# Performance work log

Hardware: AMD Instinct MI355X
Metric: run time of the kernel (lower is better)

## Reference

```python
import jax, jax.numpy as jnp
import numpy as np

HIDDEN = 2560
NUM_HEADS = 8
NUM_KV_HEADS = 1
HEAD_DIM = 512  # is_full=True -> HEAD_DIM_FULL
MAX_HD = 512
SCALE = 1.0 / float(HEAD_DIM) ** 0.5
SEQ = 32768
SLIDE = 512
CUR_POS = 4000
RING_POS = 100


def setup_inputs() -> dict:
    key = jax.random.key(0)
    ks = jax.random.split(key, 7)
    x = jax.random.normal(ks[0], (1, HIDDEN, 1, 1), jnp.float32)
    kv_full = jax.random.normal(ks[1], (2, NUM_KV_HEADS, SEQ, MAX_HD), jnp.float32) * 0.02
    kv_sliding = jax.random.normal(ks[2], (2, NUM_KV_HEADS, SLIDE, MAX_HD), jnp.float32) * 0.02
    wq = jax.random.normal(ks[3], (NUM_HEADS * HEAD_DIM, HIDDEN), jnp.float32) * 0.02
    wk = jax.random.normal(ks[4], (NUM_KV_HEADS * HEAD_DIM, HIDDEN), jnp.float32) * 0.02
    wv = jax.random.normal(ks[5], (NUM_KV_HEADS * HEAD_DIM, HIDDEN), jnp.float32) * 0.02
    wo = jax.random.normal(ks[6], (HIDDEN, NUM_HEADS * HEAD_DIM), jnp.float32) * 0.02
    return {"x": x, "kv_sliding": kv_sliding, "kv_full": kv_full,
            "wq": wq, "wk": wk, "wv": wv, "wo": wo,
            "current_pos": CUR_POS, "ring_pos": RING_POS}


def reference(x, kv_sliding, kv_full, wq, wk, wv, wo, current_pos, ring_pos):
    # 1x1 convs on a [1,C,1,1] input are plain matvecs
    xv = x.reshape(HIDDEN)
    q = (wq @ xv).reshape(NUM_HEADS, HEAD_DIM)            # [H, D]
    k = (wk @ xv).reshape(NUM_KV_HEADS, HEAD_DIM)         # [1, D]
    v = (wv @ xv).reshape(NUM_KV_HEADS, HEAD_DIM)         # [1, D]
    # is_full=True, slot_idx=0: slice-update write into kv_full at current_pos
    kv_full = jax.lax.dynamic_update_slice(
        kv_full, k[None, :, None, :].astype(kv_full.dtype), (0, 0, current_pos, 0))
    kv_full = jax.lax.dynamic_update_slice(
        kv_full, v[None, :, None, :].astype(kv_full.dtype), (1, 0, current_pos, 0))
    k_cache = kv_full[0, 0, :, :HEAD_DIM]                 # [S, D]
    v_cache = kv_full[1, 0, :, :HEAD_DIM]                 # [S, D]
    # GQA with 1 kv head: repeat == broadcast across the H query heads
    scores = jnp.einsum('hd,sd->hs', q.astype(jnp.float32),
                        k_cache.astype(jnp.float32)) * SCALE   # [H, S]
    probs = jax.nn.softmax(scores, axis=-1)
    attn = jnp.einsum('hs,sd->hd', probs,
                      v_cache.astype(jnp.float32)).astype(x.dtype)  # [H, D]
    out = (wo @ attn.reshape(NUM_HEADS * HEAD_DIM)).reshape(1, HIDDEN, 1, 1)
    return out
```

## Files before the change

### kernel.cpp

```cpp
#include <hip/hip_runtime.h>
#include <stdint.h>

#define HIDDEN 2560
#define NHEADS 8
#define HD 512
#define QDIM (NHEADS * HD)
#define SEQ 32768
#define CHUNK 64
#define NCHUNK (SEQ / CHUNK)
#define PART_ST (8 + NHEADS * HD)
#define SCALE 0.044194173824159216f

#define WS_QKV 0
#define WS_K   4096
#define WS_V   4608
#define WS_ATT 8192
#define WS_PART 16384

__global__ __launch_bounds__(256) void qkv_gemv(
    const float* __restrict__ x,
    const float* __restrict__ wq,
    const float* __restrict__ wk,
    const float* __restrict__ wv,
    float* __restrict__ qkv) {
  const int row = blockIdx.x * 4 + (threadIdx.x >> 6);
  const int lane = threadIdx.x & 63;
  const float* w;
  if (row < QDIM) w = wq + (size_t)row * HIDDEN;
  else if (row < QDIM + HD) w = wk + (size_t)(row - QDIM) * HIDDEN;
  else w = wv + (size_t)(row - QDIM - HD) * HIDDEN;
  float acc = 0.f;
#pragma unroll
  for (int i = 0; i < 5; i++) {
    const int j = i * 512 + lane * 8;
    float4 a0 = *(const float4*)(w + j);
    float4 a1 = *(const float4*)(w + j + 4);
    float4 b0 = *(const float4*)(x + j);
    float4 b1 = *(const float4*)(x + j + 4);
    acc += a0.x * b0.x + a0.y * b0.y + a0.z * b0.z + a0.w * b0.w +
           a1.x * b1.x + a1.y * b1.y + a1.z * b1.z + a1.w * b1.w;
  }
#pragma unroll
  for (int off = 32; off > 0; off >>= 1) acc += __shfl_xor(acc, off);
  if (lane == 0) qkv[row] = acc;
}

__global__ __launch_bounds__(256) void attn_partial(
    const float* __restrict__ kvfull,
    const float* __restrict__ ws,
    const int* __restrict__ cur_pos,
    float* __restrict__ part) {
  __shared__ float sc[CHUNK][NHEADS];
  __shared__ float4 vtmp[NHEADS][128];
  const int tid = threadIdx.x;
  const int lane = tid & 63;
  const int wid = tid >> 6;
  const int cur = cur_pos[0];
  const int s0 = blockIdx.x * CHUNK;
  const float* K = kvfull;
  const float* V = kvfull + (size_t)SEQ * HD;

  float qf[NHEADS][8];
#pragma unroll
  for (int h = 0; h < NHEADS; h++) {
    float4 a = *(const float4*)(ws + WS_QKV + h * HD + lane * 8);
    float4 b = *(const float4*)(ws + WS_QKV + h * HD + lane * 8 + 4);
    qf[h][0] = a.x; qf[h][1] = a.y; qf[h][2] = a.z; qf[h][3] = a.w;
    qf[h][4] = b.x; qf[h][5] = b.y; qf[h][6] = b.z; qf[h][7] = b.w;
  }

  for (int ii = 0; ii < CHUNK / 4; ii++) {
    const int scix = wid * (CHUNK / 4) + ii;
    const int s = s0 + scix;
    const float* krow = (s == cur) ? (ws + WS_K) : (K + (size_t)s * HD);
    float4 a = *(const float4*)(krow + lane * 8);
    float4 b = *(const float4*)(krow + lane * 8 + 4);
    float kb[8] = {a.x, a.y, a.z, a.w, b.x, b.y, b.z, b.w};
    float p[NHEADS];
#pragma unroll
    for (int h = 0; h < NHEADS; h++) {
      float t = 0.f;
#pragma unroll
      for (int e = 0; e < 8; e++) t += kb[e] * qf[h][e];
      p[h] = t;
    }
#pragma unroll
    for (int off = 32; off > 0; off >>= 1) {
#pragma unroll
      for (int h = 0; h < NHEADS; h++) p[h] += __shfl_xor(p[h], off);
    }
    if (lane == 0) {
#pragma unroll
      for (int h = 0; h < NHEADS; h++) sc[scix][h] = __expf(p[h] * SCALE);
    }
  }
  __syncthreads();

  float* pb = part + (size_t)blockIdx.x * PART_ST;
  if (tid < NHEADS) {
    float lsum = 0.f;
    for (int s = 0; s < CHUNK; s++) lsum += sc[s][tid];
    pb[tid] = lsum;
  }

  const int g = tid >> 7;
  const int tl = tid & 127;
  const int d0 = tl * 4;
  float4 acc[NHEADS];
#pragma unroll
  for (int h = 0; h < NHEADS; h++) acc[h] = make_float4(0.f, 0.f, 0.f, 0.f);
  for (int sy = g * (CHUNK / 2); sy < (g + 1) * (CHUNK / 2); sy++) {
    const int s = s0 + sy;
    const float* vrow = (s == cur) ? (ws + WS_V) : (V + (size_t)s * HD);
    float4 v4 = *(const float4*)(vrow + d0);
#pragma unroll
    for (int h = 0; h < NHEADS; h++) {
      const float pp = sc[sy][h];
      acc[h].x += pp * v4.x; acc[h].y += pp * v4.y;
      acc[h].z += pp * v4.z; acc[h].w += pp * v4.w;
    }
  }
  if (g == 1) {
#pragma unroll
    for (int h = 0; h < NHEADS; h++) vtmp[h][tl] = acc[h];
  }
  __syncthreads();
  if (g == 0) {
#pragma unroll
    for (int h = 0; h < NHEADS; h++) {
      float4 o = vtmp[h][tl];
      o.x += acc[h].x; o.y += acc[h].y; o.z += acc[h].z; o.w += acc[h].w;
      *(float4*)(pb + 8 + h * HD + d0) = o;
    }
  }
}

__global__ __launch_bounds__(256) void attn_reduce(
    const float* __restrict__ part,
    float* __restrict__ attn) {
  const int h = blockIdx.x >> 4;
  const int dgrp = blockIdx.x & 15;
  const int tid = threadIdx.x;
  __shared__ float red[256];
  __shared__ float pacc[8][32];

  red[tid] = part[(size_t)tid * PART_ST + h] + part[(size_t)(tid + 256) * PART_ST + h];
  __syncthreads();
  for (int off = 128; off > 0; off >>= 1) {
    if (tid < off) red[tid] += red[tid + off];
    __syncthreads();
  }
  const float Linv = 1.f / red[0];

  const int dloc = tid & 31;
  const int bs = tid >> 5;
  const int d = dgrp * 32 + dloc;
  float acc = 0.f;
#pragma unroll 8
  for (int b = bs * (NCHUNK / 8); b < (bs + 1) * (NCHUNK / 8); b++) {
    acc += part[(size_t)b * PART_ST + 8 + h * HD + d];
  }
  pacc[bs][dloc] = acc;
  __syncthreads();
  if (tid < 32) {
    float s = ((pacc[0][tid] + pacc[1][tid]) + (pacc[2][tid] + pacc[3][tid])) +
              ((pacc[4][tid] + pacc[5][tid]) + (pacc[6][tid] + pacc[7][tid]));
    attn[h * HD + dgrp * 32 + tid] = s * Linv;
  }
}

__global__ __launch_bounds__(256) void out_gemv(
    const float* __restrict__ wo,
    const float* __restrict__ attn,
    float* __restrict__ out) {
  const int row = blockIdx.x * 4 + (threadIdx.x >> 6);
  const int lane = threadIdx.x & 63;
  const float* w = wo + (size_t)row * QDIM;
  float acc = 0.f;
#pragma unroll
  for (int i = 0; i < 8; i++) {
    const int j = i * 512 + lane * 8;
    float4 w0 = *(const float4*)(w + j);
    float4 w1 = *(const float4*)(w + j + 4);
    float4 a0 = *(const float4*)(attn + j);
    float4 a1 = *(const float4*)(attn + j + 4);
    acc += w0.x * a0.x + w0.y * a0.y + w0.z * a0.z + w0.w * a0.w +
           w1.x * a1.x + w1.y * a1.y + w1.z * a1.z + w1.w * a1.w;
  }
#pragma unroll
  for (int off = 32; off > 0; off >>= 1) acc += __shfl_xor(acc, off);
  if (lane == 0) out[row] = acc;
}

extern "C" void kernel_launch(void* const* d_in, const int* in_sizes, int n_in,
                              void* d_out, int out_size, void* d_ws, size_t ws_size,
                              hipStream_t stream) {
  (void)in_sizes; (void)n_in; (void)out_size; (void)ws_size;
  const float* x      = (const float*)d_in[0];
  const float* kvfull = (const float*)d_in[2];
  const float* wq     = (const float*)d_in[3];
  const float* wk     = (const float*)d_in[4];
  const float* wv     = (const float*)d_in[5];
  const float* wo     = (const float*)d_in[6];
  const int* cur_pos  = (const int*)d_in[7];
  float* out = (float*)d_out;
  float* ws = (float*)d_ws;

  qkv_gemv<<<(QDIM + 2 * HD) / 4, 256, 0, stream>>>(x, wq, wk, wv, ws + WS_QKV);
  attn_partial<<<NCHUNK, 256, 0, stream>>>(kvfull, ws, cur_pos, ws + WS_PART);
  attn_reduce<<<NHEADS * 16, 256, 0, stream>>>(ws + WS_PART, ws + WS_ATT);
  out_gemv<<<HIDDEN / 4, 256, 0, stream>>>(wo, ws + WS_ATT, out);
}
```

Measured before the change: 282.2 us.

## Fuse four attention-decode kernels into one cooperative persistent kernel with grid syncs

```diff
diff --git a/kernel.cpp b/kernel.cpp
--- a/kernel.cpp
+++ b/kernel.cpp
@@ -1,4 +1,5 @@
 #include <hip/hip_runtime.h>
+#include <hip/hip_cooperative_groups.h>
 #include <stdint.h>
 
 #define HIDDEN 2560
@@ -6,190 +7,202 @@
 #define HD 512
 #define QDIM (NHEADS * HD)
 #define SEQ 32768
-#define CHUNK 64
+#define CHUNK 128
 #define NCHUNK (SEQ / CHUNK)
-#define PART_ST (8 + NHEADS * HD)
+#define PART_ST (8 + QDIM)
 #define SCALE 0.044194173824159216f
-
-#define WS_QKV 0
-#define WS_K   4096
-#define WS_V   4608
-#define WS_ATT 8192
+#define NBLK 256
+#define NTHR 256
+
+#define WS_Q    0
+#define WS_K    4096
+#define WS_V    4608
+#define WS_ATT  8192
 #define WS_PART 16384
 
-__global__ __launch_bounds__(256) void qkv_gemv(
+__global__ __launch_bounds__(NTHR) void fused_attn(
     const float* __restrict__ x,
+    const float* __restrict__ kvfull,
     const float* __restrict__ wq,
     const float* __restrict__ wk,
     const float* __restrict__ wv,
-    float* __restrict__ qkv) {
-  const int row = blockIdx.x * 4 + (threadIdx.x >> 6);
-  const int lane = threadIdx.x & 63;
-  const float* w;
-  if (row < QDIM) w = wq + (size_t)row * HIDDEN;
-  else if (row < QDIM + HD) w = wk + (size_t)(row - QDIM) * HIDDEN;
-  else w = wv + (size_t)(row - QDIM - HD) * HIDDEN;
-  float acc = 0.f;
-#pragma unroll
-  for (int i = 0; i < 5; i++) {
-    const int j = i * 512 + lane * 8;
-    float4 a0 = *(const float4*)(w + j);
-    float4 a1 = *(const float4*)(w + j + 4);
-    float4 b0 = *(const float4*)(x + j);
-    float4 b1 = *(const float4*)(x + j + 4);
-    acc += a0.x * b0.x + a0.y * b0.y + a0.z * b0.z + a0.w * b0.w +
-           a1.x * b1.x + a1.y * b1.y + a1.z * b1.z + a1.w * b1.w;
-  }
-#pragma unroll
-  for (int off = 32; off > 0; off >>= 1) acc += __shfl_xor(acc, off);
-  if (lane == 0) qkv[row] = acc;
-}
-
-__global__ __launch_bounds__(256) void attn_partial(
-    const float* __restrict__ kvfull,
-    const float* __restrict__ ws,
+    const float* __restrict__ wo,
     const int* __restrict__ cur_pos,
-    float* __restrict__ part) {
-  __shared__ float sc[CHUNK][NHEADS];
-  __shared__ float4 vtmp[NHEADS][128];
+    float* __restrict__ ws,
+    float* __restrict__ out) {
+  namespace cg = cooperative_groups;
+  cg::grid_group grid = cg::this_grid();
+
   const int tid = threadIdx.x;
   const int lane = tid & 63;
   const int wid = tid >> 6;
-  const int cur = cur_pos[0];
-  const int s0 = blockIdx.x * CHUNK;
-  const float* K = kvfull;
-  const float* V = kvfull + (size_t)SEQ * HD;
-
-  float qf[NHEADS][8];
-#pragma unroll
-  for (int h = 0; h < NHEADS; h++) {
-    float4 a = *(const float4*)(ws + WS_QKV + h * HD + lane * 8);
-    float4 b = *(const float4*)(ws + WS_QKV + h * HD + lane * 8 + 4);
-    qf[h][0] = a.x; qf[h][1] = a.y; qf[h][2] = a.z; qf[h][3] = a.w;
-    qf[h][4] = b.x; qf[h][5] = b.y; qf[h][6] = b.z; qf[h][7] = b.w;
-  }
-
-  for (int ii = 0; ii < CHUNK / 4; ii++) {
-    const int scix = wid * (CHUNK / 4) + ii;
-    const int s = s0 + scix;
-    const float* krow = (s == cur) ? (ws + WS_K) : (K + (size_t)s * HD);
-    float4 a = *(const float4*)(krow + lane * 8);
-    float4 b = *(const float4*)(krow + lane * 8 + 4);
-    float kb[8] = {a.x, a.y, a.z, a.w, b.x, b.y, b.z, b.w};
-    float p[NHEADS];
+  const int b = blockIdx.x;
+  const int gw = b * 4 + wid;
+
+  __shared__ float sc[CHUNK * NHEADS];
+  __shared__ float4 vtmp[NHEADS * 128];
+  __shared__ float sLinv;
+
+  for (int r = gw; r < QDIM + 2 * HD; r += 4 * NBLK) {
+    const float* w;
+    if (r < QDIM) w = wq + (size_t)r * HIDDEN;
+    else if (r < QDIM + HD) w = wk + (size_t)(r - QDIM) * HIDDEN;
+    else w = wv + (size_t)(r - QDIM - HD) * HIDDEN;
+    float acc = 0.f;
+#pragma unroll
+    for (int i = 0; i < 5; i++) {
+      const int j = i * 512 + lane * 8;
+      float4 a0 = *(const float4*)(w + j);
+      float4 a1 = *(const float4*)(w + j + 4);
+      float4 b0 = *(const float4*)(x + j);
+      float4 b1 = *(const float4*)(x + j + 4);
+      acc += a0.x * b0.x + a0.y * b0.y + a0.z * b0.z + a0.w * b0.w +
+             a1.x * b1.x + a1.y * b1.y + a1.z * b1.z + a1.w * b1.w;
+    }
+#pragma unroll
+    for (int off = 32; off > 0; off >>= 1) acc += __shfl_xor(acc, off);
+    if (lane == 0) ws[WS_Q + r] = acc;
+  }
+
+  grid.sync();
+
+  {
+    const int cur = cur_pos[0];
+    const float* K = kvfull;
+    const float* V = kvfull + (size_t)SEQ * HD;
+    const int s0 = b * CHUNK;
+
+    float qf[NHEADS][8];
 #pragma unroll
     for (int h = 0; h < NHEADS; h++) {
-      float t = 0.f;
-#pragma unroll
-      for (int e = 0; e < 8; e++) t += kb[e] * qf[h][e];
-      p[h] = t;
-    }
-#pragma unroll
-    for (int off = 32; off > 0; off >>= 1) {
-#pragma unroll
-      for (int h = 0; h < NHEADS; h++) p[h] += __shfl_xor(p[h], off);
-    }
-    if (lane == 0) {
-#pragma unroll
-      for (int h = 0; h < NHEADS; h++) sc[scix][h] = __expf(p[h] * SCALE);
-    }
-  }
-  __syncthreads();
-
-  float* pb = part + (size_t)blockIdx.x * PART_ST;
-  if (tid < NHEADS) {
-    float lsum = 0.f;
-    for (int s = 0; s < CHUNK; s++) lsum += sc[s][tid];
-    pb[tid] = lsum;
-  }
-
-  const int g = tid >> 7;
-  const int tl = tid & 127;
-  const int d0 = tl * 4;
-  float4 acc[NHEADS];
-#pragma unroll
-  for (int h = 0; h < NHEADS; h++) acc[h] = make_float4(0.f, 0.f, 0.f, 0.f);
-  for (int sy = g * (CHUNK / 2); sy < (g + 1) * (CHUNK / 2); sy++) {
-    const int s = s0 + sy;
-    const float* vrow = (s == cur) ? (ws + WS_V) : (V + (size_t)s * HD);
-    float4 v4 = *(const float4*)(vrow + d0);
-#pragma unroll
-    for (int h = 0; h < NHEADS; h++) {
-      const float pp = sc[sy][h];
-      acc[h].x += pp * v4.x; acc[h].y += pp * v4.y;
-      acc[h].z += pp * v4.z; acc[h].w += pp * v4.w;
-    }
-  }
-  if (g == 1) {
-#pragma unroll
-    for (int h = 0; h < NHEADS; h++) vtmp[h][tl] = acc[h];
-  }
-  __syncthreads();
-  if (g == 0) {
-#pragma unroll
-    for (int h = 0; h < NHEADS; h++) {
-      float4 o = vtmp[h][tl];
-      o.x += acc[h].x; o.y += acc[h].y; o.z += acc[h].z; o.w += acc[h].w;
-      *(float4*)(pb + 8 + h * HD + d0) = o;
-    }
-  }
-}
-
-__global__ __launch_bounds__(256) void attn_reduce(
-    const float* __restrict__ part,
-    float* __restrict__ attn) {
-  const int h = blockIdx.x >> 4;
-  const int dgrp = blockIdx.x & 15;
-  const int tid = threadIdx.x;
-  __shared__ float red[256];
-  __shared__ float pacc[8][32];
-
-  red[tid] = part[(size_t)tid * PART_ST + h] + part[(size_t)(tid + 256) * PART_ST + h];
-  __syncthreads();
-  for (int off = 128; off > 0; off >>= 1) {
-    if (tid < off) red[tid] += red[tid + off];
-    __syncthreads();
-  }
-  const float Linv = 1.f / red[0];
-
-  const int dloc = tid & 31;
-  const int bs = tid >> 5;
-  const int d = dgrp * 32 + dloc;
-  float acc = 0.f;
-#pragma unroll 8
-  for (int b = bs * (NCHUNK / 8); b < (bs + 1) * (NCHUNK / 8); b++) {
-    acc += part[(size_t)b * PART_ST + 8 + h * HD + d];
-  }
-  pacc[bs][dloc] = acc;
-  __syncthreads();
-  if (tid < 32) {
-    float s = ((pacc[0][tid] + pacc[1][tid]) + (pacc[2][tid] + pacc[3][tid])) +
-              ((pacc[4][tid] + pacc[5][tid]) + (pacc[6][tid] + pacc[7][tid]));
-    attn[h * HD + dgrp * 32 + tid] = s * Linv;
-  }
-}
-
-__global__ __launch_bounds__(256) void out_gemv(
-    const float* __restrict__ wo,
-    const float* __restrict__ attn,
-    float* __restrict__ out) {
-  const int row = blockIdx.x * 4 + (threadIdx.x >> 6);
-  const int lane = threadIdx.x & 63;
-  const float* w = wo + (size_t)row * QDIM;
-  float acc = 0.f;
-#pragma unroll
-  for (int i = 0; i < 8; i++) {
-    const int j = i * 512 + lane * 8;
-    float4 w0 = *(const float4*)(w + j);
-    float4 w1 = *(const float4*)(w + j + 4);
-    float4 a0 = *(const float4*)(attn + j);
-    float4 a1 = *(const float4*)(attn + j + 4);
-    acc += w0.x * a0.x + w0.y * a0.y + w0.z * a0.z + w0.w * a0.w +
-           w1.x * a1.x + w1.y * a1.y + w1.z * a1.z + w1.w * a1.w;
-  }
-#pragma unroll
-  for (int off = 32; off > 0; off >>= 1) acc += __shfl_xor(acc, off);
-  if (lane == 0) out[row] = acc;
+      float4 a = *(const float4*)(ws + WS_Q + h * HD + lane * 8);
+      float4 c = *(const float4*)(ws + WS_Q + h * HD + lane * 8 + 4);
+      qf[h][0] = a.x; qf[h][1] = a.y; qf[h][2] = a.z; qf[h][3] = a.w;
+      qf[h][4] = c.x; qf[h][5] = c.y; qf[h][6] = c.z; qf[h][7] = c.w;
+    }
+
+    for (int ii = 0; ii < CHUNK / 4; ii++) {
+      const int scix = wid * (CHUNK / 4) + ii;
+      const int s = s0 + scix;
+      const float* krow = (s == cur) ? (ws + WS_K) : (K + (size_t)s * HD);
+      float4 a = *(const float4*)(krow + lane * 8);
+      float4 c = *(const float4*)(krow + lane * 8 + 4);
+      float kb[8] = {a.x, a.y, a.z, a.w, c.x, c.y, c.z, c.w};
+      float p[NHEADS];
+#pragma unroll
+      for (int h = 0; h < NHEADS; h++) {
+        float t = 0.f;
+#pragma unroll
+        for (int e = 0; e < 8; e++) t += kb[e] * qf[h][e];
+        p[h] = t;
+      }
+#pragma unroll
+      for (int off = 32; off > 0; off >>= 1) {
+#pragma unroll
+        for (int h = 0; h < NHEADS; h++) p[h] += __shfl_xor(p[h], off);
+      }
+      if (lane == 0) {
+#pragma unroll
+        for (int h = 0; h < NHEADS; h++) sc[scix * NHEADS + h] = __expf(p[h] * SCALE);
+      }
+    }
+    __syncthreads();
+
+    float* pb = ws + WS_PART + (size_t)b * PART_ST;
+    {
+      const int h0 = wid * 2;
+      float s1 = sc[lane * NHEADS + h0]     + sc[(64 + lane) * NHEADS + h0];
+      float s2 = sc[lane * NHEADS + h0 + 1] + sc[(64 + lane) * NHEADS + h0 + 1];
+#pragma unroll
+      for (int off = 32; off > 0; off >>= 1) {
+        s1 += __shfl_xor(s1, off);
+        s2 += __shfl_xor(s2, off);
+      }
+      if (lane == 0) { pb[h0] = s1; pb[h0 + 1] = s2; }
+    }
+
+    const int g = tid >> 7;
+    const int tl = tid & 127;
+    const int d0 = tl * 4;
+    float4 acc8[NHEADS];
+#pragma unroll
+    for (int h = 0; h < NHEADS; h++) acc8[h] = make_float4(0.f, 0.f, 0.f, 0.f);
+    for (int sy = g * (CHUNK / 2); sy < (g + 1) * (CHUNK / 2); sy++) {
+      const int s = s0 + sy;
+      const float* vrow = (s == cur) ? (ws + WS_V) : (V + (size_t)s * HD);
+      float4 v4 = *(const float4*)(vrow + d0);
+#pragma unroll
+      for (int h = 0; h < NHEADS; h++) {
+        const float pp = sc[sy * NHEADS + h];
+        acc8[h].x += pp * v4.x; acc8[h].y += pp * v4.y;
+        acc8[h].z += pp * v4.z; acc8[h].w += pp * v4.w;
+      }
+    }
+    if (g == 1) {
+#pragma unroll
+      for (int h = 0; h < NHEADS; h++) vtmp[h * 128 + tl] = acc8[h];
+    }
+    __syncthreads();
+    if (g == 0) {
+#pragma unroll
+      for (int h = 0; h < NHEADS; h++) {
+        float4 o = vtmp[h * 128 + tl];
+        o.x += acc8[h].x; o.y += acc8[h].y; o.z += acc8[h].z; o.w += acc8[h].w;
+        *(float4*)(pb + 8 + h * HD + d0) = o;
+      }
+    }
+  }
+
+  grid.sync();
+
+  {
+    const int h = b >> 5;
+    const float* part = ws + WS_PART;
+    if (wid == 0) {
+      float d_ = 0.f;
+#pragma unroll
+      for (int q4 = 0; q4 < 4; q4++)
+        d_ += part[(size_t)(q4 * 64 + lane) * PART_ST + h];
+#pragma unroll
+      for (int off = 32; off > 0; off >>= 1) d_ += __shfl_xor(d_, off);
+      if (lane == 0) sLinv = 1.f / d_;
+    }
+    const int dim = tid & 15;
+    const int bg = tid >> 4;
+    const int dl = (b * 16 + dim) & (HD - 1);
+    float a_ = 0.f;
+    for (int bb = bg * 16; bb < bg * 16 + 16; bb++)
+      a_ += part[(size_t)bb * PART_ST + 8 + h * HD + dl];
+    __syncthreads();
+    sc[tid] = a_;
+    __syncthreads();
+    if (tid < 16) {
+      float s_ = 0.f;
+#pragma unroll
+      for (int q4 = 0; q4 < 16; q4++) s_ += sc[q4 * 16 + tid];
+      ws[WS_ATT + b * 16 + tid] = s_ * sLinv;
+    }
+  }
+
+  grid.sync();
+
+  for (int r = gw; r < HIDDEN; r += 4 * NBLK) {
+    const float* w = wo + (size_t)r * QDIM;
+    float acc = 0.f;
+#pragma unroll
+    for (int i = 0; i < 8; i++) {
+      const int j = i * 512 + lane * 8;
+      float4 w0 = *(const float4*)(w + j);
+      float4 w1 = *(const float4*)(w + j + 4);
+      float4 a0 = *(const float4*)(ws + WS_ATT + j);
+      float4 a1 = *(const float4*)(ws + WS_ATT + j + 4);
+      acc += w0.x * a0.x + w0.y * a0.y + w0.z * a0.z + w0.w * a0.w +
+             w1.x * a1.x + w1.y * a1.y + w1.z * a1.z + w1.w * a1.w;
+    }
+#pragma unroll
+    for (int off = 32; off > 0; off >>= 1) acc += __shfl_xor(acc, off);
+    if (lane == 0) out[r] = acc;
+  }
 }
 
 extern "C" void kernel_launch(void* const* d_in, const int* in_sizes, int n_in,
@@ -206,8 +219,8 @@
   float* out = (float*)d_out;
   float* ws = (float*)d_ws;
 
-  qkv_gemv<<<(QDIM + 2 * HD) / 4, 256, 0, stream>>>(x, wq, wk, wv, ws + WS_QKV);
-  attn_partial<<<NCHUNK, 256, 0, stream>>>(kvfull, ws, cur_pos, ws + WS_PART);
-  attn_reduce<<<NHEADS * 16, 256, 0, stream>>>(ws + WS_PART, ws + WS_ATT);
-  out_gemv<<<HIDDEN / 4, 256, 0, stream>>>(wo, ws + WS_ATT, out);
+  void* args[] = {(void*)&x, (void*)&kvfull, (void*)&wq, (void*)&wk, (void*)&wv,
+                  (void*)&wo, (void*)&cur_pos, (void*)&ws, (void*)&out};
+  hipLaunchCooperativeKernel((void*)fused_attn, dim3(NBLK), dim3(NTHR),
+                             args, 0, stream);
 }
```

New measurement: 399.0 us. +41.4%, slower.
